# Kernel optimization log

Measured on AMD Instinct MI355X. Metric: run time of the kernel, lower is better.

The kernel has to match this reference:

```python
import jax, jax.numpy as jnp
import numpy as np

B, N = 1, 768
C_S, C_Z, C_H, H, PQ, PV = 384, 128, 16, 12, 4, 8
INF, EPS = 1e5, 1e-8
SOFTPLUS_INV_1 = 0.541324854612918


def _quat_to_rot(q):
    # q: [..., 4] unit quaternions (w, x, y, z) -> [..., 3, 3]
    w, x, y, z = q[..., 0], q[..., 1], q[..., 2], q[..., 3]
    R = jnp.stack([
        1 - 2 * (y * y + z * z), 2 * (x * y - w * z), 2 * (x * z + w * y),
        2 * (x * y + w * z), 1 - 2 * (x * x + z * z), 2 * (y * z - w * x),
        2 * (x * z - w * y), 2 * (y * z + w * x), 1 - 2 * (x * x + y * y),
    ], axis=-1)
    return R.reshape(q.shape[:-1] + (3, 3))


def setup_inputs() -> dict:
    key = jax.random.key(0)
    ks = jax.random.split(key, 24)
    def lin(k, din, dout):
        return jax.random.normal(k, (din, dout), jnp.float32) / np.sqrt(din)
    quat = jax.random.normal(ks[2], (B, N, 4), jnp.float32)
    quat = quat / jnp.linalg.norm(quat, axis=-1, keepdims=True)
    return {
        "s": jax.random.normal(ks[0], (B, N, C_S), jnp.float32),
        "z": jax.random.normal(ks[1], (B, N, N, C_Z), jnp.float32),
        "rot": _quat_to_rot(quat),
        "trans": 10.0 * jax.random.normal(ks[3], (B, N, 3), jnp.float32),
        "mask": jnp.ones((B, N), jnp.float32),
        "wq": lin(ks[4], C_S, H * C_H), "bq": jnp.zeros((H * C_H,), jnp.float32),
        "wkv": lin(ks[5], C_S, 2 * H * C_H), "bkv": jnp.zeros((2 * H * C_H,), jnp.float32),
        "wqp": lin(ks[6], C_S, H * PQ * 3), "bqp": jnp.zeros((H * PQ * 3,), jnp.float32),
        "wkvp": lin(ks[7], C_S, H * (PQ + PV) * 3), "bkvp": jnp.zeros((H * (PQ + PV) * 3,), jnp.float32),
        "wb": lin(ks[8], C_Z, H), "bb": jnp.zeros((H,), jnp.float32),
        "wdz": lin(ks[9], C_Z, C_Z // 4), "bdz": jnp.zeros((C_Z // 4,), jnp.float32),
        "head_weights": jnp.full((H,), SOFTPLUS_INV_1, jnp.float32),
        "wout": lin(ks[10], H * (C_Z // 4 + C_H + PV * 4), C_S),
        "bout": jnp.zeros((C_S,), jnp.float32),
    }


def reference(s, z, rot, trans, mask, wq, bq, wkv, bkv, wqp, bqp, wkvp, bkvp,
              wb, bb, wdz, bdz, head_weights, wout, bout):
    # scalar q, k, v: [B, N, H, C_H]
    q = (s @ wq + bq).reshape(B, N, H, C_H)
    kv = (s @ wkv + bkv).reshape(B, N, H, 2 * C_H)
    k, v = kv[..., :C_H], kv[..., C_H:]

    def make_pts(w, b, npts):
        p = s @ w + b                                       # [B, N, H*npts*3]
        p = jnp.stack(jnp.split(p, 3, axis=-1), axis=-1)    # [B, N, H*npts, 3]
        p = jnp.einsum('bnxy,bnpy->bnpx', rot, p) + trans[:, :, None, :]
        return p.reshape(B, N, H, npts, 3)

    q_pts = make_pts(wqp, bqp, PQ)                          # [B, N, H, PQ, 3]
    kv_pts = make_pts(wkvp, bkvp, PQ + PV)
    k_pts, v_pts = kv_pts[..., :PQ, :], kv_pts[..., PQ:, :]

    b_bias = z @ wb + bb                                    # [B, N, N, H]
    a = jnp.einsum('bihc,bjhc->bhij', q, k) * np.sqrt(1.0 / (3 * C_H))
    a = a + np.sqrt(1.0 / 3) * jnp.transpose(b_bias, (0, 3, 1, 2))

    disp = q_pts[:, :, None] - k_pts[:, None]               # [B, i, j, H, PQ, 3]
    pt_att = jnp.sum(disp ** 2, axis=-1)                    # [B, i, j, H, PQ]
    hw = jax.nn.softplus(head_weights) * np.sqrt(1.0 / (3 * (PQ * 9.0 / 2)))
    pt_att = -0.5 * jnp.sum(pt_att * hw[:, None], axis=-1)  # [B, i, j, H]
    a = a + jnp.transpose(pt_att, (0, 3, 1, 2))

    sq_mask = INF * (mask[:, :, None] * mask[:, None, :] - 1.0)
    a = jax.nn.softmax(a + sq_mask[:, None], axis=-1)       # [B, H, i, j]

    o = jnp.einsum('bhij,bjhc->bihc', a, v).reshape(B, N, -1)
    o_pt = jnp.einsum('bhij,bjhpx->bihpx', a, v_pts)        # [B, N, H, PV, 3]
    o_pt = jnp.einsum('bixy,bihpx->bihpy', rot, o_pt - trans[:, :, None, None, :])
    o_pt_norm = jnp.sqrt(jnp.sum(o_pt ** 2, axis=-1) + EPS).reshape(B, N, -1)
    o_pt = o_pt.reshape(B, N, -1, 3)

    pair_z = z @ wdz + bdz                                  # [B, N, N, C_Z//4]
    o_pair = jnp.einsum('bhij,bijc->bihc', a, pair_z).reshape(B, N, -1)

    feats = jnp.concatenate(
        [o, o_pt[..., 0], o_pt[..., 1], o_pt[..., 2], o_pt_norm, o_pair], axis=-1)
    return feats @ wout + bout
```

## Files before the change

### kernel.cpp

```cpp
#include <hip/hip_runtime.h>
#include <hip/hip_bf16.h>
#include <math.h>

#define NTOK 768
#define CS   384
#define CZ   128
#define NH   12
#define INF_ 100000.0f
#define EPS_ 1e-8f

typedef unsigned int  uint32;
typedef unsigned short ushort;
typedef __attribute__((ext_vector_type(8))) short bf16x8;
typedef __attribute__((ext_vector_type(4))) float f32x4;

__device__ __forceinline__ float bflo(uint32 u) { return __uint_as_float((u & 0xffffu) << 16); }
__device__ __forceinline__ float bfhi(uint32 u) { return __uint_as_float(u & 0xffff0000u); }
__device__ __forceinline__ uint32 pkbf(float a, float b) {
    union { ushort s[2]; uint32 u; } r;
    __hip_bfloat16 ha = __float2bfloat16(a);
    __hip_bfloat16 hb = __float2bfloat16(b);
    __builtin_memcpy(&r.s[0], &ha, 2);
    __builtin_memcpy(&r.s[1], &hb, 2);
    return r.u;
}
__device__ __forceinline__ ushort bf16h(float x) {
    __hip_bfloat16 h = __float2bfloat16(x);
    ushort r; __builtin_memcpy(&r, &h, 2); return r;
}
__device__ __forceinline__ float bfdec(ushort u) { return __uint_as_float(((uint32)u) << 16); }

#define QK_SCALE 0.14433756729740643f
#define B_SCALE  0.5773502691896258f
#define HW_SCALE 0.13608276348795434f

__global__ __launch_bounds__(256) void k1a_gemm(
    const float* __restrict__ s,
    const float* __restrict__ wq, const float* __restrict__ wkv,
    const float* __restrict__ wqp, const float* __restrict__ wkvp,
    float* __restrict__ RAW)
{
    __shared__ float sA[32][72];
    __shared__ float sB[32][72];
    const int tid  = threadIdx.x;
    const int tok0 = blockIdx.x * 64;
    const int col0 = blockIdx.y * 64;

    const int m0 = (tid & 15) * 4;
    const int n0 = (tid >> 4) * 4;

    float4 acc[4];
    #pragma unroll
    for (int nn = 0; nn < 4; nn++) acc[nn] = make_float4(0.f, 0.f, 0.f, 0.f);

    const int lam = tid >> 2, lak = (tid & 3) * 8;
    const int lbk = tid >> 3, lbc = (tid & 7) * 8;
    const int gcol = col0 + lbc;
    const float* wsrc; int wwidth, woff;
    if (gcol < 192)      { wsrc = wq;   wwidth = 192; woff = gcol; }
    else if (gcol < 576) { wsrc = wkv;  wwidth = 384; woff = gcol - 192; }
    else if (gcol < 720) { wsrc = wqp;  wwidth = 144; woff = gcol - 576; }
    else                 { wsrc = wkvp; wwidth = 432; woff = gcol - 720; }

    for (int kb = 0; kb < CS; kb += 32) {
        const float4 a0 = *(const float4*)&s[(tok0 + lam) * CS + kb + lak];
        const float4 a1 = *(const float4*)&s[(tok0 + lam) * CS + kb + lak + 4];
        const float4 b0 = *(const float4*)&wsrc[(size_t)(kb + lbk) * wwidth + woff];
        const float4 b1 = *(const float4*)&wsrc[(size_t)(kb + lbk) * wwidth + woff + 4];
        __syncthreads();
        sA[lak + 0][lam] = a0.x; sA[lak + 1][lam] = a0.y;
        sA[lak + 2][lam] = a0.z; sA[lak + 3][lam] = a0.w;
        sA[lak + 4][lam] = a1.x; sA[lak + 5][lam] = a1.y;
        sA[lak + 6][lam] = a1.z; sA[lak + 7][lam] = a1.w;
        *(float4*)&sB[lbk][lbc]     = b0;
        *(float4*)&sB[lbk][lbc + 4] = b1;
        __syncthreads();
        #pragma unroll
        for (int k = 0; k < 32; k++) {
            const float4 av = *(const float4*)&sA[k][m0];
            const float4 bv = *(const float4*)&sB[k][n0];
            acc[0].x += av.x * bv.x; acc[0].y += av.y * bv.x; acc[0].z += av.z * bv.x; acc[0].w += av.w * bv.x;
            acc[1].x += av.x * bv.y; acc[1].y += av.y * bv.y; acc[1].z += av.z * bv.y; acc[1].w += av.w * bv.y;
            acc[2].x += av.x * bv.z; acc[2].y += av.y * bv.z; acc[2].z += av.z * bv.z; acc[2].w += av.w * bv.z;
            acc[3].x += av.x * bv.w; acc[3].y += av.y * bv.w; acc[3].z += av.z * bv.w; acc[3].w += av.w * bv.w;
        }
    }
    #pragma unroll
    for (int nn = 0; nn < 4; nn++)
        *(float4*)&RAW[(size_t)(col0 + n0 + nn) * NTOK + tok0 + m0] = acc[nn];
}

__global__ __launch_bounds__(256) void k1b_finish(
    const float* __restrict__ RAW,
    const float* __restrict__ rot, const float* __restrict__ trans,
    const float* __restrict__ bq, const float* __restrict__ bkv,
    const float* __restrict__ bqp, const float* __restrict__ bkvp,
    const float* __restrict__ head_weights,
    ushort* __restrict__ VTH, float* __restrict__ QP, ushort* __restrict__ VPTH,
    float* __restrict__ AP, ushort* __restrict__ BPH,
    float* __restrict__ RQN, float* __restrict__ CKN)
{
    __shared__ float hwS[NH];
    const int tid = threadIdx.x;
    const int t  = blockIdx.x * 16 + (tid & 15);
    const int wk = tid >> 4;

    if (tid < NH) hwS[tid] = logf(1.0f + expf(head_weights[tid])) * HW_SCALE;

    float R[9], T3[3];
    #pragma unroll
    for (int x = 0; x < 9; x++) R[x] = rot[t * 9 + x];
    #pragma unroll
    for (int x = 0; x < 3; x++) T3[x] = trans[t * 3 + x];
    __syncthreads();

    for (int col = wk; col < 192; col += 16) {
        const int h = col >> 4, c = col & 15;
        AP[(size_t)(h * 28 + c) * NTOK + t] = QK_SCALE * (RAW[(size_t)col * NTOK + t] + bq[col]);
    }
    for (int idx = wk; idx < 192; idx += 16) {
        const int h = idx >> 4, c = idx & 15;
        BPH[(size_t)(h * 28 + c) * NTOK + t] = bf16h(RAW[(size_t)(192 + h * 32 + c) * NTOK + t] + bkv[h * 32 + c]);
        VTH[(size_t)idx * NTOK + t] = bf16h(RAW[(size_t)(192 + h * 32 + 16 + c) * NTOK + t] + bkv[h * 32 + 16 + c]);
    }
    for (int pidx = wk; pidx < 48; pidx += 16) {
        const int h = pidx >> 2, p = pidx & 3;
        const float r0 = RAW[(size_t)(576 + 0 * 48 + pidx) * NTOK + t] + bqp[0 * 48 + pidx];
        const float r1 = RAW[(size_t)(576 + 1 * 48 + pidx) * NTOK + t] + bqp[1 * 48 + pidx];
        const float r2 = RAW[(size_t)(576 + 2 * 48 + pidx) * NTOK + t] + bqp[2 * 48 + pidx];
        #pragma unroll
        for (int x = 0; x < 3; x++) {
            const float v = R[x*3+0]*r0 + R[x*3+1]*r1 + R[x*3+2]*r2 + T3[x];
            QP[t * 144 + pidx * 3 + x] = v;
            AP[(size_t)(h * 28 + 16 + p * 3 + x) * NTOK + t] = hwS[h] * v;
        }
    }
    for (int pidx = wk; pidx < 144; pidx += 16) {
        const int h = pidx / 12, pp = pidx % 12;
        const float r0 = RAW[(size_t)(720 + 0 * 144 + pidx) * NTOK + t] + bkvp[0 * 144 + pidx];
        const float r1 = RAW[(size_t)(720 + 1 * 144 + pidx) * NTOK + t] + bkvp[1 * 144 + pidx];
        const float r2 = RAW[(size_t)(720 + 2 * 144 + pidx) * NTOK + t] + bkvp[2 * 144 + pidx];
        #pragma unroll
        for (int x = 0; x < 3; x++) {
            const float v = R[x*3+0]*r0 + R[x*3+1]*r1 + R[x*3+2]*r2 + T3[x];
            if (pp < 4) BPH[(size_t)(h * 28 + 16 + pp * 3 + x) * NTOK + t] = bf16h(v);
            else        VPTH[(size_t)((h * 8 + pp - 4) * 3 + x) * NTOK + t] = bf16h(v);
        }
    }
    __syncthreads();
    if (wk < NH) {
        const int h = wk;
        float sq = 0.f, sk = 0.f;
        #pragma unroll
        for (int d = 0; d < 12; d++) {
            const float a = QP[t * 144 + h * 12 + d];
            sq += a * a;
            const float b = bfdec(BPH[(size_t)(h * 28 + 16 + d) * NTOK + t]);
            sk += b * b;
        }
        RQN[h * NTOK + t] = -0.5f * hwS[h] * sq;
        CKN[h * NTOK + t] = -0.5f * hwS[h] * sk;
    }
}

__global__ __launch_bounds__(768) void k23_fused(
    const float* __restrict__ z, const float* __restrict__ wb, const float* __restrict__ bb,
    const float* __restrict__ wdz, const float* __restrict__ bdz,
    const float* __restrict__ AP, const ushort* __restrict__ BPH,
    const float* __restrict__ RQN, const float* __restrict__ CKN,
    const float* __restrict__ mask,
    const ushort* __restrict__ VTH, const ushort* __restrict__ VPTH,
    float* __restrict__ O, float* __restrict__ OPT, float* __restrict__ OPAIR)
{
    __shared__ __align__(16) uint32 sm32[(49408 + 18528) / 4];
    uint32* pzL = sm32;
    ushort* wBs = (ushort*)sm32;
    uint32* bbH = sm32 + 49408 / 4;
    __shared__ float bbS[12], bdzS[32];

    const int i = blockIdx.x, tid = threadIdx.x;
    const int h = tid >> 6;
    const int l = tid & 63;

    for (int idx = tid; idx < 48 * 64; idx += 768) {
        const int o = idx >> 6, k2 = (idx & 63) * 2;
        float f0, f1;
        if (o < 12)      { f0 = wb[k2 * 12 + o];         f1 = wb[(k2 + 1) * 12 + o]; }
        else if (o < 44) { f0 = wdz[k2 * 32 + (o - 12)]; f1 = wdz[(k2 + 1) * 32 + (o - 12)]; }
        else             { f0 = 0.f; f1 = 0.f; }
        *(uint32*)&wBs[o * 136 + k2] = pkbf(f0, f1);
    }
    if (tid < 12) bbS[tid] = bb[tid];
    else if (tid >= 32 && tid < 64) bdzS[tid - 32] = bdz[tid - 32];
    __syncthreads();

    bf16x8 Bf[3][4];
    #pragma unroll
    for (int t = 0; t < 3; t++)
        #pragma unroll
        for (int ks = 0; ks < 4; ks++)
            Bf[t][ks] = *(const bf16x8*)&wBs[(t * 16 + (l & 15)) * 136 + ks * 32 + (l >> 4) * 8];
    __syncthreads();

    const float* zb = z + ((size_t)i * NTOK + h * 64 + (l & 15)) * CZ + (l >> 4) * 8;
    float4 pa[8];
    #pragma unroll
    for (int ks = 0; ks < 4; ks++) {
        pa[2 * ks]     = *(const float4*)&zb[ks * 32];
        pa[2 * ks + 1] = *(const float4*)&zb[ks * 32 + 4];
    }

    #pragma unroll
    for (int st = 0; st < 4; st++) {
        const int jb = h * 64 + st * 16;
        union { uint32 u[4]; bf16x8 v; } Au[4];
        #pragma unroll
        for (int ks = 0; ks < 4; ks++) {
            Au[ks].u[0] = pkbf(pa[2 * ks].x,     pa[2 * ks].y);
            Au[ks].u[1] = pkbf(pa[2 * ks].z,     pa[2 * ks].w);
            Au[ks].u[2] = pkbf(pa[2 * ks + 1].x, pa[2 * ks + 1].y);
            Au[ks].u[3] = pkbf(pa[2 * ks + 1].z, pa[2 * ks + 1].w);
        }
        if (st < 3) {
            const float* zn = zb + (size_t)(st + 1) * 16 * CZ;
            #pragma unroll
            for (int ks = 0; ks < 4; ks++) {
                pa[2 * ks]     = *(const float4*)&zn[ks * 32];
                pa[2 * ks + 1] = *(const float4*)&zn[ks * 32 + 4];
            }
        }

        f32x4 acc[3];
        #pragma unroll
        for (int t = 0; t < 3; t++) acc[t] = (f32x4){0.f, 0.f, 0.f, 0.f};
        #pragma unroll
        for (int ks = 0; ks < 4; ks++)
            #pragma unroll
            for (int t = 0; t < 3; t++)
                acc[t] = __builtin_amdgcn_mfma_f32_16x16x32_bf16(Au[ks].v, Bf[t][ks], acc[t], 0, 0, 0);

        const int jq = jb + (l >> 4) * 4;
        #pragma unroll
        for (int t = 0; t < 3; t++) {
            const int o = t * 16 + (l & 15);
            if (o < 12) {
                const float bz = bbS[o];
                bbH[o * 386 + (jq >> 1)]     = pkbf(acc[t][0] + bz, acc[t][1] + bz);
                bbH[o * 386 + (jq >> 1) + 1] = pkbf(acc[t][2] + bz, acc[t][3] + bz);
            } else if (o < 44) {
                const int c = o - 12;
                const float bz = bdzS[c];
                pzL[c * 386 + (jq >> 1)]     = pkbf(acc[t][0] + bz, acc[t][1] + bz);
                pzL[c * 386 + (jq >> 1) + 1] = pkbf(acc[t][2] + bz, acc[t][3] + bz);
            }
        }
    }
    __syncthreads();

    float ap[28];
    #pragma unroll
    for (int k = 0; k < 28; k++) ap[k] = AP[(size_t)(h * 28 + k) * NTOK + i];
    const float rq = RQN[h * NTOK + i];
    const float mi = mask[i];

    f32x4 lg[3];
    #pragma unroll
    for (int qb = 0; qb < 3; qb++) {
        const int j4 = qb * 256 + l * 4;
        const float4 ck  = *(const float4*)&CKN[h * NTOK + j4];
        const uint32 bx = bbH[h * 386 + (j4 >> 1)];
        const uint32 by = bbH[h * 386 + (j4 >> 1) + 1];
        const float4 mj  = *(const float4*)&mask[j4];
        f32x4 a;
        a[0] = B_SCALE * bflo(bx) + rq + ck.x + INF_ * (mi * mj.x - 1.0f);
        a[1] = B_SCALE * bfhi(bx) + rq + ck.y + INF_ * (mi * mj.y - 1.0f);
        a[2] = B_SCALE * bflo(by) + rq + ck.z + INF_ * (mi * mj.z - 1.0f);
        a[3] = B_SCALE * bfhi(by) + rq + ck.w + INF_ * (mi * mj.w - 1.0f);
        #pragma unroll
        for (int k = 0; k < 28; k++) {
            const uint2 u = *(const uint2*)&BPH[(size_t)(h * 28 + k) * NTOK + j4];
            a[0] += ap[k] * bflo(u.x); a[1] += ap[k] * bfhi(u.x);
            a[2] += ap[k] * bflo(u.y); a[3] += ap[k] * bfhi(u.y);
        }
        lg[qb] = a;
    }

    float m = -3.0e38f;
    #pragma unroll
    for (int qb = 0; qb < 3; qb++)
        #pragma unroll
        for (int v = 0; v < 4; v++) m = fmaxf(m, lg[qb][v]);
    #pragma unroll
    for (int off = 32; off >= 1; off >>= 1) m = fmaxf(m, __shfl_xor(m, off));
    float ssum = 0.0f;
    #pragma unroll
    for (int qb = 0; qb < 3; qb++)
        #pragma unroll
        for (int v = 0; v < 4; v++) {
            const float e = __expf(lg[qb][v] - m);
            lg[qb][v] = e;
            ssum += e;
        }
    #pragma unroll
    for (int off = 32; off >= 1; off >>= 1) ssum += __shfl_xor(ssum, off);
    const float inv = 1.0f / ssum;
    #pragma unroll
    for (int qb = 0; qb < 3; qb++)
        #pragma unroll
        for (int v = 0; v < 4; v++) lg[qb][v] *= inv;

    #pragma unroll 2
    for (int r = 0; r < 40; r++) {
        const ushort* srcH = (r < 16) ? &VTH[(size_t)(h * 16 + r) * NTOK]
                                      : &VPTH[(size_t)(h * 24 + (r - 16)) * NTOK];
        const uint2* s2 = (const uint2*)srcH;
        const uint2 u0 = s2[l], u1 = s2[64 + l], u2 = s2[128 + l];
        float acc = lg[0][0]*bflo(u0.x) + lg[0][1]*bfhi(u0.x) + lg[0][2]*bflo(u0.y) + lg[0][3]*bfhi(u0.y)
                  + lg[1][0]*bflo(u1.x) + lg[1][1]*bfhi(u1.x) + lg[1][2]*bflo(u1.y) + lg[1][3]*bfhi(u1.y)
                  + lg[2][0]*bflo(u2.x) + lg[2][1]*bfhi(u2.x) + lg[2][2]*bflo(u2.y) + lg[2][3]*bfhi(u2.y);
        #pragma unroll
        for (int off = 32; off >= 1; off >>= 1) acc += __shfl_xor(acc, off);
        if (l == 0) {
            if (r < 16) O[i * 192 + h * 16 + r] = acc;
            else        OPT[i * 288 + h * 24 + (r - 16)] = acc;
        }
    }
    #pragma unroll 2
    for (int c = 0; c < 32; c++) {
        float a = 0.f;
        #pragma unroll
        for (int it = 0; it < 3; it++) {
            const uint32* p2 = &pzL[c * 386 + it * 128 + 2 * l];
            const uint32 ux = p2[0], uy = p2[1];
            a += lg[it][0] * bflo(ux) + lg[it][1] * bfhi(ux)
               + lg[it][2] * bflo(uy) + lg[it][3] * bfhi(uy);
        }
        #pragma unroll
        for (int off = 32; off >= 1; off >>= 1) a += __shfl_xor(a, off);
        if (l == 0) OPAIR[i * 384 + h * 32 + c] = a;
    }
}

#define K4T 8
__global__ __launch_bounds__(256) void k4_out(
    const float* __restrict__ O, const float* __restrict__ OPT, const float* __restrict__ OPAIR,
    const float* __restrict__ rot, const float* __restrict__ trans,
    const float* __restrict__ wout, const float* __restrict__ bout,
    float* __restrict__ out)
{
    __shared__ float f[K4T][960];
    const int n0 = blockIdx.x * K4T, tid = threadIdx.x;

    for (int idx = tid; idx < K4T * 192; idx += 256) {
        const int t = idx / 192, k = idx % 192;
        f[t][k] = O[(n0 + t) * 192 + k];
    }
    for (int idx = tid; idx < K4T * 384; idx += 256) {
        const int t = idx / 384, k = idx % 384;
        f[t][576 + k] = OPAIR[(n0 + t) * 384 + k];
    }
    for (int idx = tid; idx < K4T * 96; idx += 256) {
        const int t = idx / 96, hp = idx % 96;
        const int n = n0 + t;
        const float vx = OPT[n * 288 + hp * 3 + 0] - trans[n * 3 + 0];
        const float vy = OPT[n * 288 + hp * 3 + 1] - trans[n * 3 + 1];
        const float vz = OPT[n * 288 + hp * 3 + 2] - trans[n * 3 + 2];
        const float o0 = rot[n*9+0]*vx + rot[n*9+3]*vy + rot[n*9+6]*vz;
        const float o1 = rot[n*9+1]*vx + rot[n*9+4]*vy + rot[n*9+7]*vz;
        const float o2 = rot[n*9+2]*vx + rot[n*9+5]*vy + rot[n*9+8]*vz;
        f[t][192 + hp] = o0;
        f[t][288 + hp] = o1;
        f[t][384 + hp] = o2;
        f[t][480 + hp] = sqrtf(o0*o0 + o1*o1 + o2*o2 + EPS_);
    }
    __syncthreads();

    for (int o = tid; o < 384; o += 256) {
        float acc[K4T];
        #pragma unroll
        for (int t = 0; t < K4T; t++) acc[t] = bout[o];
        for (int kq = 0; kq < 240; kq++) {
            float4 fv[K4T];
            #pragma unroll
            for (int t = 0; t < K4T; t++) fv[t] = *(const float4*)&f[t][kq * 4];
            #pragma unroll
            for (int kk = 0; kk < 4; kk++) {
                const float wv = wout[(kq * 4 + kk) * 384 + o];
                #pragma unroll
                for (int t = 0; t < K4T; t++) {
                    const float fe = (kk == 0) ? fv[t].x : (kk == 1) ? fv[t].y
                                   : (kk == 2) ? fv[t].z : fv[t].w;
                    acc[t] += fe * wv;
                }
            }
        }
        #pragma unroll
        for (int t = 0; t < K4T; t++) out[(n0 + t) * 384 + o] = acc[t];
    }
}

extern "C" void kernel_launch(void* const* d_in, const int* in_sizes, int n_in,
                              void* d_out, int out_size, void* d_ws, size_t ws_size,
                              hipStream_t stream) {
    (void)in_sizes; (void)n_in; (void)out_size; (void)ws_size;
    const float* s     = (const float*)d_in[0];
    const float* z     = (const float*)d_in[1];
    const float* rot   = (const float*)d_in[2];
    const float* trans = (const float*)d_in[3];
    const float* mask  = (const float*)d_in[4];
    const float* wq    = (const float*)d_in[5];
    const float* bq    = (const float*)d_in[6];
    const float* wkv   = (const float*)d_in[7];
    const float* bkv   = (const float*)d_in[8];
    const float* wqp   = (const float*)d_in[9];
    const float* bqp   = (const float*)d_in[10];
    const float* wkvp  = (const float*)d_in[11];
    const float* bkvp  = (const float*)d_in[12];
    const float* wb    = (const float*)d_in[13];
    const float* bb    = (const float*)d_in[14];
    const float* wdz   = (const float*)d_in[15];
    const float* bdz   = (const float*)d_in[16];
    const float* hwts  = (const float*)d_in[17];
    const float* wout  = (const float*)d_in[18];
    const float* bout  = (const float*)d_in[19];
    float* out = (float*)d_out;

    float* ws = (float*)d_ws;
    ushort* VTH  = (ushort*)ws;
    ushort* VPTH = (ushort*)(ws + 73728);
    float* QP    = ws + 73728 + 110592;
    float* O     = QP  + 110592;
    float* OPT   = O   + 147456;
    float* OPAIR = OPT + 221184;
    float* RAW   = OPAIR + 294912;
    float* AP    = RAW + 884736;
    ushort* BPH  = (ushort*)(AP + 258048);
    float* RQN   = AP + 258048 + 129024;
    float* CKN   = RQN + 9216;

    hipLaunchKernelGGL(k1a_gemm, dim3(NTOK / 64, 1152 / 64), dim3(256), 0, stream,
                       s, wq, wkv, wqp, wkvp, RAW);
    hipLaunchKernelGGL(k1b_finish, dim3(NTOK / 16), dim3(256), 0, stream,
                       RAW, rot, trans, bq, bkv, bqp, bkvp, hwts,
                       VTH, QP, VPTH, AP, BPH, RQN, CKN);
    hipLaunchKernelGGL(k23_fused, dim3(NTOK), dim3(768), 0, stream,
                       z, wb, bb, wdz, bdz,
                       AP, BPH, RQN, CKN, mask, VTH, VPTH,
                       O, OPT, OPAIR);
    hipLaunchKernelGGL(k4_out, dim3(NTOK / K4T), dim3(256), 0, stream,
                       O, OPT, OPAIR, rot, trans, wout, bout, out);
}
```

Before: 323.0 us.

## Shrink k23 block to 8 waves and spill pair projection to global scratch

The fused bias/attention kernel now runs with 512 threads (8 waves) instead of 768. Each wave handles 96 j-rows of the z projection, and the per-head softmax/aggregation loop is strided over 12 heads. The 32-channel pair projection no longer lives in LDS and is written to a global workspace buffer (PZB), then read back for the o_pair reduction. The smaller LDS footprint and block size are meant to let more blocks sit on each CU, at the cost of extra global traffic and uneven head work across waves (4 waves process two heads).

Measured after the change: 389.2 us. 20.5% more time.

```diff
diff --git a/kernel.cpp b/kernel.cpp
--- a/kernel.cpp
+++ b/kernel.cpp
@@ -163,26 +163,25 @@
     }
 }
 
-__global__ __launch_bounds__(768) void k23_fused(
+__global__ __launch_bounds__(512) void k23_fused(
     const float* __restrict__ z, const float* __restrict__ wb, const float* __restrict__ bb,
     const float* __restrict__ wdz, const float* __restrict__ bdz,
     const float* __restrict__ AP, const ushort* __restrict__ BPH,
     const float* __restrict__ RQN, const float* __restrict__ CKN,
     const float* __restrict__ mask,
     const ushort* __restrict__ VTH, const ushort* __restrict__ VPTH,
+    uint32* __restrict__ PZB,
     float* __restrict__ O, float* __restrict__ OPT, float* __restrict__ OPAIR)
 {
-    __shared__ __align__(16) uint32 sm32[(49408 + 18528) / 4];
-    uint32* pzL = sm32;
-    ushort* wBs = (ushort*)sm32;
-    uint32* bbH = sm32 + 49408 / 4;
+    __shared__ __align__(16) ushort wBs[48 * 136];
+    __shared__ uint32 bbH[12 * 386];
     __shared__ float bbS[12], bdzS[32];
 
     const int i = blockIdx.x, tid = threadIdx.x;
-    const int h = tid >> 6;
+    const int w = tid >> 6;
     const int l = tid & 63;
 
-    for (int idx = tid; idx < 48 * 64; idx += 768) {
+    for (int idx = tid; idx < 48 * 64; idx += 512) {
         const int o = idx >> 6, k2 = (idx & 63) * 2;
         float f0, f1;
         if (o < 12)      { f0 = wb[k2 * 12 + o];         f1 = wb[(k2 + 1) * 12 + o]; }
@@ -200,9 +199,8 @@
         #pragma unroll
         for (int ks = 0; ks < 4; ks++)
             Bf[t][ks] = *(const bf16x8*)&wBs[(t * 16 + (l & 15)) * 136 + ks * 32 + (l >> 4) * 8];
-    __syncthreads();
-
-    const float* zb = z + ((size_t)i * NTOK + h * 64 + (l & 15)) * CZ + (l >> 4) * 8;
+
+    const float* zb = z + ((size_t)i * NTOK + w * 96 + (l & 15)) * CZ + (l >> 4) * 8;
     float4 pa[8];
     #pragma unroll
     for (int ks = 0; ks < 4; ks++) {
@@ -211,8 +209,8 @@
     }
 
     #pragma unroll
-    for (int st = 0; st < 4; st++) {
-        const int jb = h * 64 + st * 16;
+    for (int st = 0; st < 6; st++) {
+        const int jb = w * 96 + st * 16;
         union { uint32 u[4]; bf16x8 v; } Au[4];
         #pragma unroll
         for (int ks = 0; ks < 4; ks++) {
@@ -221,7 +219,7 @@
             Au[ks].u[2] = pkbf(pa[2 * ks + 1].x, pa[2 * ks + 1].y);
             Au[ks].u[3] = pkbf(pa[2 * ks + 1].z, pa[2 * ks + 1].w);
         }
-        if (st < 3) {
+        if (st < 5) {
             const float* zn = zb + (size_t)(st + 1) * 16 * CZ;
             #pragma unroll
             for (int ks = 0; ks < 4; ks++) {
@@ -250,94 +248,96 @@
             } else if (o < 44) {
                 const int c = o - 12;
                 const float bz = bdzS[c];
-                pzL[c * 386 + (jq >> 1)]     = pkbf(acc[t][0] + bz, acc[t][1] + bz);
-                pzL[c * 386 + (jq >> 1) + 1] = pkbf(acc[t][2] + bz, acc[t][3] + bz);
+                PZB[(size_t)(i * 32 + c) * 384 + (jq >> 1)]     = pkbf(acc[t][0] + bz, acc[t][1] + bz);
+                PZB[(size_t)(i * 32 + c) * 384 + (jq >> 1) + 1] = pkbf(acc[t][2] + bz, acc[t][3] + bz);
             }
         }
     }
     __syncthreads();
 
-    float ap[28];
-    #pragma unroll
-    for (int k = 0; k < 28; k++) ap[k] = AP[(size_t)(h * 28 + k) * NTOK + i];
-    const float rq = RQN[h * NTOK + i];
-    const float mi = mask[i];
-
-    f32x4 lg[3];
-    #pragma unroll
-    for (int qb = 0; qb < 3; qb++) {
-        const int j4 = qb * 256 + l * 4;
-        const float4 ck  = *(const float4*)&CKN[h * NTOK + j4];
-        const uint32 bx = bbH[h * 386 + (j4 >> 1)];
-        const uint32 by = bbH[h * 386 + (j4 >> 1) + 1];
-        const float4 mj  = *(const float4*)&mask[j4];
-        f32x4 a;
-        a[0] = B_SCALE * bflo(bx) + rq + ck.x + INF_ * (mi * mj.x - 1.0f);
-        a[1] = B_SCALE * bfhi(bx) + rq + ck.y + INF_ * (mi * mj.y - 1.0f);
-        a[2] = B_SCALE * bflo(by) + rq + ck.z + INF_ * (mi * mj.z - 1.0f);
-        a[3] = B_SCALE * bfhi(by) + rq + ck.w + INF_ * (mi * mj.w - 1.0f);
-        #pragma unroll
-        for (int k = 0; k < 28; k++) {
-            const uint2 u = *(const uint2*)&BPH[(size_t)(h * 28 + k) * NTOK + j4];
-            a[0] += ap[k] * bflo(u.x); a[1] += ap[k] * bfhi(u.x);
-            a[2] += ap[k] * bflo(u.y); a[3] += ap[k] * bfhi(u.y);
-        }
-        lg[qb] = a;
-    }
-
-    float m = -3.0e38f;
-    #pragma unroll
-    for (int qb = 0; qb < 3; qb++)
-        #pragma unroll
-        for (int v = 0; v < 4; v++) m = fmaxf(m, lg[qb][v]);
-    #pragma unroll
-    for (int off = 32; off >= 1; off >>= 1) m = fmaxf(m, __shfl_xor(m, off));
-    float ssum = 0.0f;
-    #pragma unroll
-    for (int qb = 0; qb < 3; qb++)
-        #pragma unroll
-        for (int v = 0; v < 4; v++) {
-            const float e = __expf(lg[qb][v] - m);
-            lg[qb][v] = e;
-            ssum += e;
-        }
-    #pragma unroll
-    for (int off = 32; off >= 1; off >>= 1) ssum += __shfl_xor(ssum, off);
-    const float inv = 1.0f / ssum;
-    #pragma unroll
-    for (int qb = 0; qb < 3; qb++)
-        #pragma unroll
-        for (int v = 0; v < 4; v++) lg[qb][v] *= inv;
-
-    #pragma unroll 2
-    for (int r = 0; r < 40; r++) {
-        const ushort* srcH = (r < 16) ? &VTH[(size_t)(h * 16 + r) * NTOK]
-                                      : &VPTH[(size_t)(h * 24 + (r - 16)) * NTOK];
-        const uint2* s2 = (const uint2*)srcH;
-        const uint2 u0 = s2[l], u1 = s2[64 + l], u2 = s2[128 + l];
-        float acc = lg[0][0]*bflo(u0.x) + lg[0][1]*bfhi(u0.x) + lg[0][2]*bflo(u0.y) + lg[0][3]*bfhi(u0.y)
-                  + lg[1][0]*bflo(u1.x) + lg[1][1]*bfhi(u1.x) + lg[1][2]*bflo(u1.y) + lg[1][3]*bfhi(u1.y)
-                  + lg[2][0]*bflo(u2.x) + lg[2][1]*bfhi(u2.x) + lg[2][2]*bflo(u2.y) + lg[2][3]*bfhi(u2.y);
-        #pragma unroll
-        for (int off = 32; off >= 1; off >>= 1) acc += __shfl_xor(acc, off);
-        if (l == 0) {
-            if (r < 16) O[i * 192 + h * 16 + r] = acc;
-            else        OPT[i * 288 + h * 24 + (r - 16)] = acc;
-        }
-    }
-    #pragma unroll 2
-    for (int c = 0; c < 32; c++) {
-        float a = 0.f;
-        #pragma unroll
-        for (int it = 0; it < 3; it++) {
-            const uint32* p2 = &pzL[c * 386 + it * 128 + 2 * l];
-            const uint32 ux = p2[0], uy = p2[1];
-            a += lg[it][0] * bflo(ux) + lg[it][1] * bfhi(ux)
-               + lg[it][2] * bflo(uy) + lg[it][3] * bfhi(uy);
-        }
-        #pragma unroll
-        for (int off = 32; off >= 1; off >>= 1) a += __shfl_xor(a, off);
-        if (l == 0) OPAIR[i * 384 + h * 32 + c] = a;
+    for (int h = w; h < 12; h += 8) {
+        float ap[28];
+        #pragma unroll
+        for (int k = 0; k < 28; k++) ap[k] = AP[(size_t)(h * 28 + k) * NTOK + i];
+        const float rq = RQN[h * NTOK + i];
+        const float mi = mask[i];
+
+        f32x4 lg[3];
+        #pragma unroll
+        for (int qb = 0; qb < 3; qb++) {
+            const int j4 = qb * 256 + l * 4;
+            const float4 ck  = *(const float4*)&CKN[h * NTOK + j4];
+            const uint32 bx = bbH[h * 386 + (j4 >> 1)];
+            const uint32 by = bbH[h * 386 + (j4 >> 1) + 1];
+            const float4 mj  = *(const float4*)&mask[j4];
+            f32x4 a;
+            a[0] = B_SCALE * bflo(bx) + rq + ck.x + INF_ * (mi * mj.x - 1.0f);
+            a[1] = B_SCALE * bfhi(bx) + rq + ck.y + INF_ * (mi * mj.y - 1.0f);
+            a[2] = B_SCALE * bflo(by) + rq + ck.z + INF_ * (mi * mj.z - 1.0f);
+            a[3] = B_SCALE * bfhi(by) + rq + ck.w + INF_ * (mi * mj.w - 1.0f);
+            #pragma unroll
+            for (int k = 0; k < 28; k++) {
+                const uint2 u = *(const uint2*)&BPH[(size_t)(h * 28 + k) * NTOK + j4];
+                a[0] += ap[k] * bflo(u.x); a[1] += ap[k] * bfhi(u.x);
+                a[2] += ap[k] * bflo(u.y); a[3] += ap[k] * bfhi(u.y);
+            }
+            lg[qb] = a;
+        }
+
+        float m = -3.0e38f;
+        #pragma unroll
+        for (int qb = 0; qb < 3; qb++)
+            #pragma unroll
+            for (int v = 0; v < 4; v++) m = fmaxf(m, lg[qb][v]);
+        #pragma unroll
+        for (int off = 32; off >= 1; off >>= 1) m = fmaxf(m, __shfl_xor(m, off));
+        float ssum = 0.0f;
+        #pragma unroll
+        for (int qb = 0; qb < 3; qb++)
+            #pragma unroll
+            for (int v = 0; v < 4; v++) {
+                const float e = __expf(lg[qb][v] - m);
+                lg[qb][v] = e;
+                ssum += e;
+            }
+        #pragma unroll
+        for (int off = 32; off >= 1; off >>= 1) ssum += __shfl_xor(ssum, off);
+        const float inv = 1.0f / ssum;
+        #pragma unroll
+        for (int qb = 0; qb < 3; qb++)
+            #pragma unroll
+            for (int v = 0; v < 4; v++) lg[qb][v] *= inv;
+
+        #pragma unroll 2
+        for (int r = 0; r < 40; r++) {
+            const ushort* srcH = (r < 16) ? &VTH[(size_t)(h * 16 + r) * NTOK]
+                                          : &VPTH[(size_t)(h * 24 + (r - 16)) * NTOK];
+            const uint2* s2 = (const uint2*)srcH;
+            const uint2 u0 = s2[l], u1 = s2[64 + l], u2 = s2[128 + l];
+            float acc = lg[0][0]*bflo(u0.x) + lg[0][1]*bfhi(u0.x) + lg[0][2]*bflo(u0.y) + lg[0][3]*bfhi(u0.y)
+                      + lg[1][0]*bflo(u1.x) + lg[1][1]*bfhi(u1.x) + lg[1][2]*bflo(u1.y) + lg[1][3]*bfhi(u1.y)
+                      + lg[2][0]*bflo(u2.x) + lg[2][1]*bfhi(u2.x) + lg[2][2]*bflo(u2.y) + lg[2][3]*bfhi(u2.y);
+            #pragma unroll
+            for (int off = 32; off >= 1; off >>= 1) acc += __shfl_xor(acc, off);
+            if (l == 0) {
+                if (r < 16) O[i * 192 + h * 16 + r] = acc;
+                else        OPT[i * 288 + h * 24 + (r - 16)] = acc;
+            }
+        }
+        #pragma unroll 2
+        for (int c = 0; c < 32; c++) {
+            const uint2* src = (const uint2*)&PZB[(size_t)(i * 32 + c) * 384];
+            float a = 0.f;
+            #pragma unroll
+            for (int it = 0; it < 3; it++) {
+                const uint2 u = src[it * 64 + l];
+                a += lg[it][0] * bflo(u.x) + lg[it][1] * bfhi(u.x)
+                   + lg[it][2] * bflo(u.y) + lg[it][3] * bfhi(u.y);
+            }
+            #pragma unroll
+            for (int off = 32; off >= 1; off >>= 1) a += __shfl_xor(a, off);
+            if (l == 0) OPAIR[i * 384 + h * 32 + c] = a;
+        }
     }
 }
 
@@ -437,15 +437,16 @@
     ushort* BPH  = (ushort*)(AP + 258048);
     float* RQN   = AP + 258048 + 129024;
     float* CKN   = RQN + 9216;
+    uint32* PZB  = (uint32*)(CKN + 9216);
 
     hipLaunchKernelGGL(k1a_gemm, dim3(NTOK / 64, 1152 / 64), dim3(256), 0, stream,
                        s, wq, wkv, wqp, wkvp, RAW);
     hipLaunchKernelGGL(k1b_finish, dim3(NTOK / 16), dim3(256), 0, stream,
                        RAW, rot, trans, bq, bkv, bqp, bkvp, hwts,
                        VTH, QP, VPTH, AP, BPH, RQN, CKN);
-    hipLaunchKernelGGL(k23_fused, dim3(NTOK), dim3(768), 0, stream,
+    hipLaunchKernelGGL(k23_fused, dim3(NTOK), dim3(512), 0, stream,
                        z, wb, bb, wdz, bdz,
-                       AP, BPH, RQN, CKN, mask, VTH, VPTH,
+                       AP, BPH, RQN, CKN, mask, VTH, VPTH, PZB,
                        O, OPT, OPAIR);
     hipLaunchKernelGGL(k4_out, dim3(NTOK / K4T), dim3(256), 0, stream,
                        O, OPT, OPAIR, rot, trans, wout, bout, out);
```
